# Optimization experiments

Measured on AMD Instinct MI355X. Metric: run time of the kernel, lower is better.

The kernel has to match this reference:

```python
import jax, jax.numpy as jnp
import numpy as np

B, NQ, NK = 16, 512, 1024
CQ, CV = 128, 128
H, D = 8, 64            # nb_heads, attention_size
SCALE = float(np.sqrt(D))


def setup_inputs() -> dict:
    key = jax.random.key(0)
    ks = jax.random.split(key, 10)
    s = 0.02
    return {
        "query": jax.random.normal(ks[0], (B, NQ, CQ), jnp.float32),
        "key": jax.random.normal(ks[1], (B, NK, CV), jnp.float32),
        "c_mask": jax.random.randint(ks[2], (B, NK), 0, 2).astype(jnp.float32),
        # torch Linear params, stored as [in, out] so y = x @ W + b
        "Wq": jax.random.normal(ks[3], (CQ, H * D), jnp.float32) * s,
        "bq": jnp.zeros((H * D,), jnp.float32),
        "Wk": jax.random.normal(ks[4], (CV, H * D), jnp.float32) * s,
        "bk": jnp.zeros((H * D,), jnp.float32),
        "Wv": jax.random.normal(ks[5], (CV, H * D), jnp.float32) * s,
        "bv": jnp.zeros((H * D,), jnp.float32),
    }


def reference(query, key, c_mask, Wq, bq, Wk, bk, Wv, bv):
    # projections -> [B, N, H, D]
    q = (query @ Wq + bq).reshape(B, NQ, H, D)
    k = (key @ Wk + bk).reshape(B, NK, H, D)
    v = (key @ Wv + bv).reshape(B, NK, H, D)
    # scaled scores [B, H, NQ, NK]
    scores = jnp.einsum('bqhd,bkhd->bhqk', q / SCALE, k)
    # additive mask: c_mask [B, NK] broadcasts over heads and queries
    scores = scores - 100000.0 * (1.0 - c_mask[:, None, None, :])
    attn = jax.nn.softmax(scores, axis=-1)
    # weighted values -> [B, NQ, H, D] -> concat heads
    c = jnp.einsum('bhqk,bkhd->bqhd', attn, v)
    return c.reshape(B, NQ, H * D)
```

## Files before the change

kernel.cpp:

```cpp
#include <hip/hip_runtime.h>
#include <hip/hip_bf16.h>

#define B_  16
#define NQ_ 512
#define NK_ 1024
#define CQ_ 128
#define H_  8
#define D_  64
#define HD_ 512

typedef __attribute__((ext_vector_type(8))) short short8;
typedef __attribute__((ext_vector_type(4))) float floatx4;

__device__ __forceinline__ short f2bf(float f) {
    union { float f; unsigned u; } x; x.f = f;
    unsigned r = (x.u + 0x7fffu + ((x.u >> 16) & 1u)) >> 16;
    return (short)r;
}
__device__ __forceinline__ int f2bf_pk(float a, float b) {
    __hip_bfloat162 h = __float22bfloat162_rn(make_float2(a, b));
    int r; __builtin_memcpy(&r, &h, 4); return r;
}
__device__ __forceinline__ short8 pack8(float4 a, float4 b) {
    union { int4 i; short8 s; } u;
    u.i = make_int4(f2bf_pk(a.x, a.y), f2bf_pk(a.z, a.w),
                    f2bf_pk(b.x, b.y), f2bf_pk(b.z, b.w));
    return u.s;
}
__device__ __forceinline__ int2 packi2(floatx4 a) {
    return make_int2(f2bf_pk(a[0], a[1]), f2bf_pk(a[2], a[3]));
}
__device__ __forceinline__ void async16(const short* g, short* l) {
    __builtin_amdgcn_global_load_lds(
        (const __attribute__((address_space(1))) void*)g,
        (__attribute__((address_space(3))) void*)l, 16, 0, 0);
}

__global__ __launch_bounds__(256) void prep_kernel(
    const float* __restrict__ W0, const float* __restrict__ W1,
    const float* __restrict__ W2, short* __restrict__ T0,
    short* __restrict__ T1, short* __restrict__ T2,
    const float* __restrict__ bq, float* __restrict__ bqs, float qscale,
    const float* __restrict__ cmask, int* __restrict__ idx,
    float* __restrict__ cm2, int* __restrict__ npad)
{
    const int blk = blockIdx.x, t = threadIdx.x;
    if (blk == 48) {
        bqs[t]       = bq[t] * qscale;
        bqs[t + 256] = bq[t + 256] * qscale;
        return;
    }
    if (blk >= 49) {
        __shared__ int wsum[4];
        const int b = blk - 49;
        const int w = t >> 6, lane = t & 63;
        float4 m4 = *(const float4*)(cmask + b * NK_ + t * 4);
        const int m0 = m4.x > 0.5f, m1 = m4.y > 0.5f, m2 = m4.z > 0.5f, m3 = m4.w > 0.5f;
        const int s = m0 + m1 + m2 + m3;
        int v = s;
        #pragma unroll
        for (int off = 1; off < 64; off <<= 1) {
            int u = __shfl_up(v, off);
            if (lane >= off) v += u;
        }
        if (lane == 63) wsum[w] = v;
        __syncthreads();
        int pre = 0;
        #pragma unroll
        for (int i = 0; i < 4; ++i) if (i < w) pre += wsum[i];
        int pos = pre + v - s;
        const int base = b * NK_;
        if (m0) { idx[base + pos] = t * 4 + 0; cm2[base + pos] = 1.0f; ++pos; }
        if (m1) { idx[base + pos] = t * 4 + 1; cm2[base + pos] = 1.0f; ++pos; }
        if (m2) { idx[base + pos] = t * 4 + 2; cm2[base + pos] = 1.0f; ++pos; }
        if (m3) { idx[base + pos] = t * 4 + 3; cm2[base + pos] = 1.0f; ++pos; }
        const int total = wsum[0] + wsum[1] + wsum[2] + wsum[3];
        for (int j = total + t; j < NK_; j += 256) {
            idx[base + j] = 0; cm2[base + j] = 0.0f;
        }
        if (t == 0) npad[b] = (total + 127) & ~127;
        return;
    }
    __shared__ short tsh[32 * 132];
    const int mat = blk >> 4, nb = blk & 15;
    const float* W = mat == 0 ? W0 : (mat == 1 ? W1 : W2);
    short* T = mat == 0 ? T0 : (mat == 1 ? T1 : T2);
    const float s = mat == 0 ? qscale : 1.0f;
    #pragma unroll
    for (int i = 0; i < 4; ++i) {
        const int i2 = i * 256 + t;
        const int k = i2 >> 3, c = (i2 & 7) * 4;
        float4 v = *(const float4*)(W + (size_t)k * HD_ + nb * 32 + c);
        tsh[(c + 0) * 132 + k] = f2bf(v.x * s);
        tsh[(c + 1) * 132 + k] = f2bf(v.y * s);
        tsh[(c + 2) * 132 + k] = f2bf(v.z * s);
        tsh[(c + 3) * 132 + k] = f2bf(v.w * s);
    }
    __syncthreads();
    #pragma unroll
    for (int j = 0; j < 2; ++j) {
        const int i2 = j * 256 + t;
        const int n = i2 >> 4, seg = (i2 & 15) * 8;
        *(short8*)(T + (size_t)(nb * 32 + n) * CQ_ + seg) =
            *(const short8*)&tsh[n * 132 + seg];
    }
}

__global__ __launch_bounds__(256, 2) void kvproj_kernel(
    const float* __restrict__ key_,
    const short* __restrict__ wkt, const short* __restrict__ wvt,
    const float* __restrict__ bk, const float* __restrict__ bv,
    short* __restrict__ ks, short* __restrict__ vt,
    const int* __restrict__ idx, const int* __restrict__ npad)
{
    __shared__ __align__(16) short csh[9216];

    int bx = blockIdx.x;
    const short* Wt; const float* bias; short* out; int transposed;
    if (bx < 128) { Wt = wkt; bias = bk; out = ks; transposed = 0; }
    else { bx -= 128; Wt = wvt; bias = bv; out = vt; transposed = 1; }

    const int mbase = bx * 128;
    const int b  = mbase >> 10;
    const int r0 = mbase & 1023;
    if (r0 >= npad[b]) return;

    const int tid  = threadIdx.x;
    const int w    = tid >> 6, lane = tid & 63;
    const int l15  = lane & 15, quad = lane >> 4;
    const int* ib = idx + b * NK_;

    short8 afr[2][4];
    #pragma unroll
    for (int mt = 0; mt < 2; ++mt) {
        const int krow = ib[r0 + w * 32 + mt * 16 + l15];
        const float* xrow = key_ + (size_t)(b * NK_ + krow) * CQ_;
        #pragma unroll
        for (int kt = 0; kt < 4; ++kt)
            afr[mt][kt] = pack8(*(const float4*)(xrow + kt * 32 + quad * 8),
                                *(const float4*)(xrow + kt * 32 + quad * 8 + 4));
    }

    #pragma unroll
    for (int hh = 0; hh < 4; ++hh) {
        const int h = blockIdx.y * 4 + hh;
        short8 bfr[4][4];
        #pragma unroll
        for (int nt = 0; nt < 4; ++nt) {
            const short8* wrow = (const short8*)(Wt + (size_t)(h * 64 + nt * 16 + l15) * CQ_);
            #pragma unroll
            for (int kt = 0; kt < 4; ++kt) bfr[nt][kt] = wrow[kt * 4 + quad];
        }
        floatx4 acc[2][4];
        #pragma unroll
        for (int mt = 0; mt < 2; ++mt)
            #pragma unroll
            for (int nt = 0; nt < 4; ++nt) {
                floatx4 a = {0.f, 0.f, 0.f, 0.f};
                #pragma unroll
                for (int kt = 0; kt < 4; ++kt)
                    a = __builtin_amdgcn_mfma_f32_16x16x32_bf16(afr[mt][kt], bfr[nt][kt], a, 0, 0, 0);
                acc[mt][nt] = a;
            }
        __syncthreads();
        #pragma unroll
        for (int mt = 0; mt < 2; ++mt)
            #pragma unroll
            for (int nt = 0; nt < 4; ++nt) {
                const float bvv = bias[h * 64 + nt * 16 + l15];
                #pragma unroll
                for (int i = 0; i < 4; ++i) {
                    const short s = f2bf(acc[mt][nt][i] + bvv);
                    const int m = w * 32 + mt * 16 + quad * 4 + i;
                    const int n = nt * 16 + l15;
                    if (!transposed) csh[m * 72 + n]  = s;
                    else             csh[n * 136 + m] = s;
                }
            }
        __syncthreads();

        const size_t bh = (size_t)(b * H_ + h);
        if (!transposed) {
            short* dst = out + (bh * NK_ + r0) * D_;
            #pragma unroll
            for (int it = 0; it < 4; ++it) {
                const int i2 = it * 256 + tid;
                const int row = i2 >> 3, c8 = (i2 & 7) * 8;
                *(short8*)(dst + i2 * 8) = *(const short8*)&csh[row * 72 + c8];
            }
        } else {
            short* dst = out + bh * D_ * NK_ + r0;
            #pragma unroll
            for (int it = 0; it < 4; ++it) {
                const int i2 = it * 256 + tid;
                const int row = i2 >> 4, c8 = (i2 & 15) * 8;
                *(short8*)(dst + (size_t)row * NK_ + c8) = *(const short8*)&csh[row * 136 + c8];
            }
        }
    }
}

__global__ __launch_bounds__(256, 2) void attn_kernel(
    const float* __restrict__ query, const short* __restrict__ ks,
    const short* __restrict__ vt, const float* __restrict__ cm2,
    const short* __restrict__ wqt, const float* __restrict__ bqs,
    const int* __restrict__ npad, float* __restrict__ out)
{
    __shared__ __align__(16) short kbuf[2][64 * 64];
    __shared__ __align__(16) short vbuf[2][64 * 64];
    __shared__ __align__(16) short psh[128 * 64];

    const int tid = threadIdx.x;
    const int w = tid >> 6, lane = tid & 63;
    const int l15 = lane & 15, quad = lane >> 4;

    const int bx   = blockIdx.x;
    const int bh_i = bx & 127;
    const int qq   = bx >> 7;
    const int h    = bh_i & 7;
    const int b    = bh_i >> 3;

    const size_t bh = (size_t)bh_i;
    const short* kb_ = ks + bh * NK_ * D_;
    const short* vb  = vt + bh * D_ * NK_;
    const float* mk  = cm2 + (size_t)b * NK_;
    const int nc = npad[b] >> 6;

    short8 qa[2][2];
    {
        short8 waf[4][4];
        #pragma unroll
        for (int dt = 0; dt < 4; ++dt)
            #pragma unroll
            for (int kt = 0; kt < 4; ++kt)
                waf[dt][kt] = *(const short8*)(wqt + (size_t)(h * 64 + dt * 16 + l15) * CQ_ + kt * 32 + quad * 8);
        const int qr0 = qq * 128 + w * 32;
        #pragma unroll
        for (int g = 0; g < 2; ++g) {
            const float* qrow = query + ((size_t)b * NQ_ + qr0 + g * 16 + l15) * CQ_;
            short8 bqf[4];
            #pragma unroll
            for (int kt = 0; kt < 4; ++kt)
                bqf[kt] = pack8(*(const float4*)(qrow + kt * 32 + quad * 8),
                                *(const float4*)(qrow + kt * 32 + quad * 8 + 4));
            const int prow = w * 32 + g * 16 + l15;
            #pragma unroll
            for (int dt = 0; dt < 4; ++dt) {
                float4 bi = *(const float4*)(bqs + h * 64 + dt * 16 + quad * 4);
                floatx4 a = {bi.x, bi.y, bi.z, bi.w};
                #pragma unroll
                for (int kt = 0; kt < 4; ++kt)
                    a = __builtin_amdgcn_mfma_f32_16x16x32_bf16(waf[dt][kt], bqf[kt], a, 0, 0, 0);
                const int c16 = (dt * 2 + (quad >> 1)) ^ (prow & 7);
                *(int2*)&psh[prow * 64 + c16 * 8 + (quad & 1) * 4] = packi2(a);
            }
            qa[g][0] = *(const short8*)&psh[prow * 64 + ((quad    ) ^ (prow & 7)) * 8];
            qa[g][1] = *(const short8*)&psh[prow * 64 + ((4 + quad) ^ (prow & 7)) * 8];
        }
    }

    const int srow8 = lane >> 3, sc = lane & 7;
    auto stage = [&](int kb0, short* kdst, short* vdst) {
        #pragma unroll
        for (int j = 0; j < 2; ++j) {
            const int row = w * 16 + j * 8 + srow8;
            const int cs = sc ^ (row & 7);
            async16(kb_ + (size_t)(kb0 + row) * D_ + cs * 8, &kdst[(w * 16 + j * 8) * 64]);
            async16(vb + (size_t)row * NK_ + kb0 + cs * 8, &vdst[(w * 16 + j * 8) * 64]);
        }
    };

    float l_lane[2] = {0.f, 0.f};
    floatx4 o_acc[2][4];
    #pragma unroll
    for (int g = 0; g < 2; ++g)
        #pragma unroll
        for (int dt = 0; dt < 4; ++dt) o_acc[g][dt] = (floatx4){0.f, 0.f, 0.f, 0.f};

    stage(0, kbuf[0], vbuf[0]);
    __syncthreads();

    for (int t = 0; t < nc; ++t) {
        const int cur = t & 1;
        if (t + 1 < nc) stage((t + 1) * 64, kbuf[cur ^ 1], vbuf[cur ^ 1]);
        const short* kb  = kbuf[cur];
        const short* vbl = vbuf[cur];
        const int kbase = t * 64;

        short8 ka[4][2];
        #pragma unroll
        for (int nt = 0; nt < 4; ++nt) {
            const int row = nt * 16 + l15;
            ka[nt][0] = *(const short8*)&kb[row * 64 + ((quad    ) ^ (row & 7)) * 8];
            ka[nt][1] = *(const short8*)&kb[row * 64 + ((4 + quad) ^ (row & 7)) * 8];
        }
        short8 vf[2][4];
        #pragma unroll
        for (int dt = 0; dt < 4; ++dt) {
            const int row = dt * 16 + l15;
            vf[0][dt] = *(const short8*)&vbl[row * 64 + ((quad    ) ^ (row & 7)) * 8];
            vf[1][dt] = *(const short8*)&vbl[row * 64 + ((4 + quad) ^ (row & 7)) * 8];
        }
        float4 m4[4];
        #pragma unroll
        for (int nt = 0; nt < 4; ++nt)
            m4[nt] = *(const float4*)(mk + kbase + nt * 16 + quad * 4);

        #pragma unroll
        for (int g = 0; g < 2; ++g) {
            floatx4 st[4];
            #pragma unroll
            for (int nt = 0; nt < 4; ++nt) {
                floatx4 a = {0.f, 0.f, 0.f, 0.f};
                a = __builtin_amdgcn_mfma_f32_16x16x32_bf16(ka[nt][1], qa[g][1], a, 0, 0, 0);
                a = __builtin_amdgcn_mfma_f32_16x16x32_bf16(ka[nt][0], qa[g][0], a, 0, 0, 0);
                st[nt] = a;
            }
            const int prow = w * 32 + g * 16 + l15;
            float psum = 0.f;
            #pragma unroll
            for (int nt = 0; nt < 4; ++nt) {
                float p0 = m4[nt].x * __builtin_amdgcn_exp2f(st[nt][0]);
                float p1 = m4[nt].y * __builtin_amdgcn_exp2f(st[nt][1]);
                float p2 = m4[nt].z * __builtin_amdgcn_exp2f(st[nt][2]);
                float p3 = m4[nt].w * __builtin_amdgcn_exp2f(st[nt][3]);
                psum += (p0 + p1) + (p2 + p3);
                int2 pk = make_int2(f2bf_pk(p0, p1), f2bf_pk(p2, p3));
                const int c16 = (2 * nt + (quad >> 1)) ^ (prow & 7);
                *(int2*)&psh[prow * 64 + c16 * 8 + (quad & 1) * 4] = pk;
            }
            l_lane[g] += psum;
            #pragma unroll
            for (int kt = 0; kt < 2; ++kt) {
                short8 pa = *(const short8*)&psh[prow * 64 + ((kt * 4 + quad) ^ (prow & 7)) * 8];
                #pragma unroll
                for (int dt = 0; dt < 4; ++dt)
                    o_acc[g][dt] = __builtin_amdgcn_mfma_f32_16x16x32_bf16(vf[kt][dt], pa, o_acc[g][dt], 0, 0, 0);
            }
        }
        __syncthreads();
    }

    #pragma unroll
    for (int g = 0; g < 2; ++g) {
        float ls = l_lane[g];
        ls += __shfl_xor(ls, 16);
        ls += __shfl_xor(ls, 32);
        const float linv = 1.0f / ls;
        const int qr = qq * 128 + w * 32 + g * 16 + l15;
        float* orow = out + ((size_t)b * NQ_ + qr) * HD_ + h * D_;
        #pragma unroll
        for (int dt = 0; dt < 4; ++dt) {
            float4 v = make_float4(o_acc[g][dt][0] * linv, o_acc[g][dt][1] * linv,
                                   o_acc[g][dt][2] * linv, o_acc[g][dt][3] * linv);
            *(float4*)(orow + dt * 16 + quad * 4) = v;
        }
    }
}

extern "C" void kernel_launch(void* const* d_in, const int* in_sizes, int n_in,
                              void* d_out, int out_size, void* d_ws, size_t ws_size,
                              hipStream_t stream) {
    const float* query = (const float*)d_in[0];
    const float* key   = (const float*)d_in[1];
    const float* cmask = (const float*)d_in[2];
    const float* Wq    = (const float*)d_in[3];
    const float* bq    = (const float*)d_in[4];
    const float* Wk    = (const float*)d_in[5];
    const float* bk    = (const float*)d_in[6];
    const float* Wv    = (const float*)d_in[7];
    const float* bv    = (const float*)d_in[8];
    float* out = (float*)d_out;

    char* ws = (char*)d_ws;
    short* ks  = (short*)(ws);
    short* vt  = (short*)(ws + (size_t)(16u << 20));
    char*  w32 = ws + (size_t)(32u << 20);
    short* wqt = (short*)(w32);
    short* wkt = (short*)(w32 + 131072);
    short* wvt = (short*)(w32 + 131072 * 2);
    float* bqs = (float*)(w32 + 131072 * 3);
    int*   idx = (int*)(w32 + 131072 * 3 + 4096);
    float* cm2 = (float*)(w32 + 131072 * 3 + 4096 + 65536);
    int*  npad = (int*)(w32 + 131072 * 3 + 4096 + 131072);

    const float qscale = 0.125f * 1.44269504f;
    prep_kernel<<<dim3(65), dim3(256), 0, stream>>>(
        Wq, Wk, Wv, wqt, wkt, wvt, bq, bqs, qscale, cmask, idx, cm2, npad);

    kvproj_kernel<<<dim3(256, 2), dim3(256), 0, stream>>>(
        key, wkt, wvt, bk, bv, ks, vt, idx, npad);

    attn_kernel<<<dim3(512), dim3(256), 0, stream>>>(
        query, ks, vt, cm2, wqt, bqs, npad, out);
}
```

Measured before the change: 136.7 us.

## Fuse K/V projection into attention kernel, computing K/V tiles on the fly

Removes the separate kvproj kernel and its global K/V round trip. Each attention block now gathers compacted key rows, projects them through the per-head Wk (staged in LDS) and Wv (held in registers), and writes bf16 K/V tiles straight into the LDS double buffers before running the attention tile. The cost is redundant projection work: each (b,h) is recomputed by all 4 query-block CTAs. It also brings extra LDS (wk_lds), more register pressure, and synchronous fp32 key loads in place of async LDS loads.

```diff
diff --git a/kernel.cpp b/kernel.cpp
--- a/kernel.cpp
+++ b/kernel.cpp
@@ -29,11 +29,6 @@
 }
 __device__ __forceinline__ int2 packi2(floatx4 a) {
     return make_int2(f2bf_pk(a[0], a[1]), f2bf_pk(a[2], a[3]));
-}
-__device__ __forceinline__ void async16(const short* g, short* l) {
-    __builtin_amdgcn_global_load_lds(
-        (const __attribute__((address_space(1))) void*)g,
-        (__attribute__((address_space(3))) void*)l, 16, 0, 0);
 }
 
 __global__ __launch_bounds__(256) void prep_kernel(
@@ -106,106 +101,15 @@
     }
 }
 
-__global__ __launch_bounds__(256, 2) void kvproj_kernel(
-    const float* __restrict__ key_,
-    const short* __restrict__ wkt, const short* __restrict__ wvt,
-    const float* __restrict__ bk, const float* __restrict__ bv,
-    short* __restrict__ ks, short* __restrict__ vt,
-    const int* __restrict__ idx, const int* __restrict__ npad)
-{
-    __shared__ __align__(16) short csh[9216];
-
-    int bx = blockIdx.x;
-    const short* Wt; const float* bias; short* out; int transposed;
-    if (bx < 128) { Wt = wkt; bias = bk; out = ks; transposed = 0; }
-    else { bx -= 128; Wt = wvt; bias = bv; out = vt; transposed = 1; }
-
-    const int mbase = bx * 128;
-    const int b  = mbase >> 10;
-    const int r0 = mbase & 1023;
-    if (r0 >= npad[b]) return;
-
-    const int tid  = threadIdx.x;
-    const int w    = tid >> 6, lane = tid & 63;
-    const int l15  = lane & 15, quad = lane >> 4;
-    const int* ib = idx + b * NK_;
-
-    short8 afr[2][4];
-    #pragma unroll
-    for (int mt = 0; mt < 2; ++mt) {
-        const int krow = ib[r0 + w * 32 + mt * 16 + l15];
-        const float* xrow = key_ + (size_t)(b * NK_ + krow) * CQ_;
-        #pragma unroll
-        for (int kt = 0; kt < 4; ++kt)
-            afr[mt][kt] = pack8(*(const float4*)(xrow + kt * 32 + quad * 8),
-                                *(const float4*)(xrow + kt * 32 + quad * 8 + 4));
-    }
-
-    #pragma unroll
-    for (int hh = 0; hh < 4; ++hh) {
-        const int h = blockIdx.y * 4 + hh;
-        short8 bfr[4][4];
-        #pragma unroll
-        for (int nt = 0; nt < 4; ++nt) {
-            const short8* wrow = (const short8*)(Wt + (size_t)(h * 64 + nt * 16 + l15) * CQ_);
-            #pragma unroll
-            for (int kt = 0; kt < 4; ++kt) bfr[nt][kt] = wrow[kt * 4 + quad];
-        }
-        floatx4 acc[2][4];
-        #pragma unroll
-        for (int mt = 0; mt < 2; ++mt)
-            #pragma unroll
-            for (int nt = 0; nt < 4; ++nt) {
-                floatx4 a = {0.f, 0.f, 0.f, 0.f};
-                #pragma unroll
-                for (int kt = 0; kt < 4; ++kt)
-                    a = __builtin_amdgcn_mfma_f32_16x16x32_bf16(afr[mt][kt], bfr[nt][kt], a, 0, 0, 0);
-                acc[mt][nt] = a;
-            }
-        __syncthreads();
-        #pragma unroll
-        for (int mt = 0; mt < 2; ++mt)
-            #pragma unroll
-            for (int nt = 0; nt < 4; ++nt) {
-                const float bvv = bias[h * 64 + nt * 16 + l15];
-                #pragma unroll
-                for (int i = 0; i < 4; ++i) {
-                    const short s = f2bf(acc[mt][nt][i] + bvv);
-                    const int m = w * 32 + mt * 16 + quad * 4 + i;
-                    const int n = nt * 16 + l15;
-                    if (!transposed) csh[m * 72 + n]  = s;
-                    else             csh[n * 136 + m] = s;
-                }
-            }
-        __syncthreads();
-
-        const size_t bh = (size_t)(b * H_ + h);
-        if (!transposed) {
-            short* dst = out + (bh * NK_ + r0) * D_;
-            #pragma unroll
-            for (int it = 0; it < 4; ++it) {
-                const int i2 = it * 256 + tid;
-                const int row = i2 >> 3, c8 = (i2 & 7) * 8;
-                *(short8*)(dst + i2 * 8) = *(const short8*)&csh[row * 72 + c8];
-            }
-        } else {
-            short* dst = out + bh * D_ * NK_ + r0;
-            #pragma unroll
-            for (int it = 0; it < 4; ++it) {
-                const int i2 = it * 256 + tid;
-                const int row = i2 >> 4, c8 = (i2 & 15) * 8;
-                *(short8*)(dst + (size_t)row * NK_ + c8) = *(const short8*)&csh[row * 136 + c8];
-            }
-        }
-    }
-}
-
-__global__ __launch_bounds__(256, 2) void attn_kernel(
-    const float* __restrict__ query, const short* __restrict__ ks,
-    const short* __restrict__ vt, const float* __restrict__ cm2,
-    const short* __restrict__ wqt, const float* __restrict__ bqs,
+__global__ __launch_bounds__(256, 2) void fused_attn(
+    const float* __restrict__ query, const float* __restrict__ key_,
+    const short* __restrict__ wqt, const short* __restrict__ wkt,
+    const short* __restrict__ wvt, const float* __restrict__ bk,
+    const float* __restrict__ bv, const float* __restrict__ bqs,
+    const int* __restrict__ idx, const float* __restrict__ cm2,
     const int* __restrict__ npad, float* __restrict__ out)
 {
+    __shared__ __align__(16) short wk_lds[64 * 128];
     __shared__ __align__(16) short kbuf[2][64 * 64];
     __shared__ __align__(16) short vbuf[2][64 * 64];
     __shared__ __align__(16) short psh[128 * 64];
@@ -220,11 +124,31 @@
     const int h    = bh_i & 7;
     const int b    = bh_i >> 3;
 
-    const size_t bh = (size_t)bh_i;
-    const short* kb_ = ks + bh * NK_ * D_;
-    const short* vb  = vt + bh * D_ * NK_;
-    const float* mk  = cm2 + (size_t)b * NK_;
-    const int nc = npad[b] >> 6;
+    const float* mk = cm2 + (size_t)b * NK_;
+    const int*   ib = idx + b * NK_;
+    const int    nc = npad[b] >> 6;
+
+    {
+        const short* wkg = wkt + (size_t)(h * 64) * CQ_;
+        #pragma unroll
+        for (int i = 0; i < 4; ++i) {
+            const int i2 = i * 256 + tid;
+            const int row = i2 >> 4, c = i2 & 15;
+            *(short8*)&wk_lds[row * 128 + ((c ^ (row & 7)) * 8)] =
+                *(const short8*)(wkg + (size_t)row * CQ_ + c * 8);
+        }
+    }
+    short8 wvf[4][4];
+    #pragma unroll
+    for (int dt = 0; dt < 4; ++dt)
+        #pragma unroll
+        for (int kt = 0; kt < 4; ++kt)
+            wvf[dt][kt] = *(const short8*)(wvt + (size_t)(h * 64 + dt * 16 + l15) * CQ_ + kt * 32 + quad * 8);
+    float bkf[4]; float4 bvf[4];
+    #pragma unroll
+    for (int nt = 0; nt < 4; ++nt) bkf[nt] = bk[h * 64 + nt * 16 + l15];
+    #pragma unroll
+    for (int dt = 0; dt < 4; ++dt) bvf[dt] = *(const float4*)(bv + h * 64 + dt * 16 + quad * 4);
 
     short8 qa[2][2];
     {
@@ -258,17 +182,19 @@
             qa[g][1] = *(const short8*)&psh[prow * 64 + ((4 + quad) ^ (prow & 7)) * 8];
         }
     }
-
-    const int srow8 = lane >> 3, sc = lane & 7;
-    auto stage = [&](int kb0, short* kdst, short* vdst) {
-        #pragma unroll
-        for (int j = 0; j < 2; ++j) {
-            const int row = w * 16 + j * 8 + srow8;
-            const int cs = sc ^ (row & 7);
-            async16(kb_ + (size_t)(kb0 + row) * D_ + cs * 8, &kdst[(w * 16 + j * 8) * 64]);
-            async16(vb + (size_t)row * NK_ + kb0 + cs * 8, &vdst[(w * 16 + j * 8) * 64]);
+    __syncthreads();
+
+    float4 kr[8];
+    auto gather = [&](int kbase) {
+        const int krow = ib[kbase + w * 16 + l15];
+        const float* xrow = key_ + (size_t)(b * NK_ + krow) * CQ_;
+        #pragma unroll
+        for (int kt = 0; kt < 4; ++kt) {
+            kr[kt * 2]     = *(const float4*)(xrow + kt * 32 + quad * 8);
+            kr[kt * 2 + 1] = *(const float4*)(xrow + kt * 32 + quad * 8 + 4);
         }
     };
+    gather(0);
 
     float l_lane[2] = {0.f, 0.f};
     floatx4 o_acc[2][4];
@@ -277,12 +203,48 @@
         #pragma unroll
         for (int dt = 0; dt < 4; ++dt) o_acc[g][dt] = (floatx4){0.f, 0.f, 0.f, 0.f};
 
-    stage(0, kbuf[0], vbuf[0]);
-    __syncthreads();
-
     for (int t = 0; t < nc; ++t) {
         const int cur = t & 1;
-        if (t + 1 < nc) stage((t + 1) * 64, kbuf[cur ^ 1], vbuf[cur ^ 1]);
+        short* kwr = kbuf[cur];
+        short* vwr = vbuf[cur];
+
+        short8 afr[4];
+        #pragma unroll
+        for (int kt = 0; kt < 4; ++kt) afr[kt] = pack8(kr[kt * 2], kr[kt * 2 + 1]);
+        if (t + 1 < nc) gather((t + 1) * 64);
+
+        #pragma unroll
+        for (int nt = 0; nt < 4; ++nt) {
+            floatx4 a = {0.f, 0.f, 0.f, 0.f};
+            #pragma unroll
+            for (int kt = 0; kt < 4; ++kt) {
+                const int row = nt * 16 + l15;
+                short8 bfr = *(const short8*)&wk_lds[row * 128 + (((kt * 4 + quad) ^ (row & 7)) * 8)];
+                a = __builtin_amdgcn_mfma_f32_16x16x32_bf16(afr[kt], bfr, a, 0, 0, 0);
+            }
+            #pragma unroll
+            for (int i = 0; i < 4; ++i) {
+                const int krw = w * 16 + quad * 4 + i;
+                const int cc = (nt * 2 + (l15 >> 3)) ^ (krw & 7);
+                kwr[krw * 64 + cc * 8 + (l15 & 7)] = f2bf(a[i] + bkf[nt]);
+            }
+        }
+        #pragma unroll
+        for (int dt = 0; dt < 4; ++dt) {
+            floatx4 a = {0.f, 0.f, 0.f, 0.f};
+            #pragma unroll
+            for (int kt = 0; kt < 4; ++kt)
+                a = __builtin_amdgcn_mfma_f32_16x16x32_bf16(wvf[dt][kt], afr[kt], a, 0, 0, 0);
+            const float* bvp = &bvf[dt].x;
+            #pragma unroll
+            for (int i = 0; i < 4; ++i) {
+                const int dr = dt * 16 + quad * 4 + i;
+                const int cc = (w * 2 + (l15 >> 3)) ^ (dr & 7);
+                vwr[dr * 64 + cc * 8 + (l15 & 7)] = f2bf(a[i] + bvp[i]);
+            }
+        }
+        __syncthreads();
+
         const short* kb  = kbuf[cur];
         const short* vbl = vbuf[cur];
         const int kbase = t * 64;
@@ -338,7 +300,6 @@
                     o_acc[g][dt] = __builtin_amdgcn_mfma_f32_16x16x32_bf16(vf[kt][dt], pa, o_acc[g][dt], 0, 0, 0);
             }
         }
-        __syncthreads();
     }
 
     #pragma unroll
@@ -373,24 +334,18 @@
     float* out = (float*)d_out;
 
     char* ws = (char*)d_ws;
-    short* ks  = (short*)(ws);
-    short* vt  = (short*)(ws + (size_t)(16u << 20));
-    char*  w32 = ws + (size_t)(32u << 20);
-    short* wqt = (short*)(w32);
-    short* wkt = (short*)(w32 + 131072);
-    short* wvt = (short*)(w32 + 131072 * 2);
-    float* bqs = (float*)(w32 + 131072 * 3);
-    int*   idx = (int*)(w32 + 131072 * 3 + 4096);
-    float* cm2 = (float*)(w32 + 131072 * 3 + 4096 + 65536);
-    int*  npad = (int*)(w32 + 131072 * 3 + 4096 + 131072);
+    short* wqt = (short*)(ws);
+    short* wkt = (short*)(ws + 131072);
+    short* wvt = (short*)(ws + 131072 * 2);
+    float* bqs = (float*)(ws + 131072 * 3);
+    int*   idx = (int*)(ws + 131072 * 3 + 4096);
+    float* cm2 = (float*)(ws + 131072 * 3 + 4096 + 65536);
+    int*  npad = (int*)(ws + 131072 * 3 + 4096 + 131072);
 
     const float qscale = 0.125f * 1.44269504f;
     prep_kernel<<<dim3(65), dim3(256), 0, stream>>>(
         Wq, Wk, Wv, wqt, wkt, wvt, bq, bqs, qscale, cmask, idx, cm2, npad);
 
-    kvproj_kernel<<<dim3(256, 2), dim3(256), 0, stream>>>(
-        key, wkt, wvt, bk, bv, ks, vt, idx, npad);
-
-    attn_kernel<<<dim3(512), dim3(256), 0, stream>>>(
-        query, ks, vt, cm2, wqt, bqs, npad, out);
-}
+    fused_attn<<<dim3(512), dim3(256), 0, stream>>>(
+        query, key, wqt, wkt, wvt, bk, bv, bqs, idx, cm2, npad, out);
+}
```

After: 167.7 us. 1.23x slower.
